# Performance work log

Hardware: AMD Instinct MI355X
Metric: run time of the kernel (lower is better)

Reference implementation:

```python
import jax, jax.numpy as jnp
import numpy as np

C = 64
G = 4          # group_number
K = 3          # kernel_size
R = 4          # reduction_ratio -> bottleneck C//R = 16
BN_EPS = 1e-3  # keras BatchNormalization default epsilon


def setup_inputs() -> dict:
    key = jax.random.key(0)
    ks = jax.random.split(key, 8)
    B, H, W = 8, 192, 192
    cr = C // R
    x = jax.random.normal(ks[0], (B, H, W, C), dtype=jnp.float32)
    # kernel_gen: Conv2D 1x1 (C -> C//R), BN, ReLU, Conv2D 1x1 (C//R -> K*K*G)
    w1 = jax.random.normal(ks[1], (C, cr), dtype=jnp.float32) * (1.0 / np.sqrt(C))
    b1 = jnp.zeros((cr,), dtype=jnp.float32)
    gamma = 1.0 + 0.1 * jax.random.normal(ks[2], (cr,), dtype=jnp.float32)
    beta = 0.1 * jax.random.normal(ks[3], (cr,), dtype=jnp.float32)
    mean = 0.1 * jax.random.normal(ks[4], (cr,), dtype=jnp.float32)
    var = jax.random.uniform(ks[5], (cr,), dtype=jnp.float32, minval=0.5, maxval=1.5)
    w2 = jax.random.normal(ks[6], (cr, K * K * G), dtype=jnp.float32) * (1.0 / np.sqrt(cr))
    b2 = jnp.zeros((K * K * G,), dtype=jnp.float32)
    return {"x": x, "w1": w1, "b1": b1, "gamma": gamma, "beta": beta,
            "mean": mean, "var": var, "w2": w2, "b2": b2}


def reference(x, w1, b1, gamma, beta, mean, var, w2, b2):
    B, H, W, Cc = x.shape
    # --- kernel generation (stride=1 -> identity pooling) ---
    t = jnp.einsum('bhwc,cd->bhwd', x, w1) + b1                 # [B,H,W,C//R]
    t = (t - mean) * jax.lax.rsqrt(var + BN_EPS) * gamma + beta  # BN (inference)
    t = jax.nn.relu(t)
    kern = jnp.einsum('bhwd,de->bhwe', t, w2) + b2               # [B,H,W,K*K*G]
    kern = kern.reshape(B, H, W, K * K, 1, G)
    # --- unfold: tf.image.extract_patches SAME, stride 1, patch order (ki,kj,C) ---
    pad = K // 2
    xp = jnp.pad(x, ((0, 0), (pad, pad), (pad, pad), (0, 0)))
    patches = jnp.stack(
        [xp[:, i:i + H, j:j + W, :] for i in range(K) for j in range(K)],
        axis=3)                                                  # [B,H,W,K*K,C]
    unfolded = patches.reshape(B, H, W, K * K, Cc // G, G)
    # --- per-pixel multiply-reduce over patch axis ---
    out = jnp.sum(kern * unfolded, axis=3)                       # [B,H,W,C//G,G]
    return out.reshape(B, H, W, Cc)
```

## Files before the change

kernel.cpp:

```cpp
#include <hip/hip_runtime.h>


#define B_   8
#define H_   192
#define W_   192
#define C_   64
#define CR_  16
#define TH_  8
#define TW_  16
#define TILES_X (W_/TW_)
#define TILES_Y (H_/TH_)
#define TILES_PER_IMG (TILES_X * TILES_Y)
#define NBLK (B_ * TILES_PER_IMG)
#define NPIX (TH_ * TW_)

constexpr float BN_EPS = 1e-3f;

template <bool INTERIOR>
__device__ __forceinline__ void phase_b(const float* __restrict__ x,
                                        float* __restrict__ out,
                                        const float4* __restrict__ s_kern,
                                        int img, int th0, int tw0, int tid)
{
    const int c4i  = tid & 15;
    const int prow = tid >> 4;
    const float* ximg = x + ((size_t)img * H_ * W_ << 6);
    float* oimg = out + ((size_t)img * H_ * W_ << 6);

    #pragma unroll 2
    for (int i = 0; i < 16; ++i) {
        const int q = i * 8 + prow;
        const int r = q >> 4, cc = q & 15;
        const int h = th0 + r, w = tw0 + cc;
        const float4* kq = &s_kern[q * 9];

        float4 acc = make_float4(0.f, 0.f, 0.f, 0.f);
        #pragma unroll
        for (int ti = 0; ti < 3; ++ti) {
            const int hh = h + ti - 1;
            int hc = hh;
            bool vh = true;
            if (!INTERIOR) {
                vh = (unsigned)hh < (unsigned)H_;
                hc = hh < 0 ? 0 : (hh >= H_ ? H_ - 1 : hh);
            }
            #pragma unroll
            for (int tj = 0; tj < 3; ++tj) {
                const int ww = w + tj - 1;
                int wc = ww;
                bool valid = true;
                if (!INTERIOR) {
                    valid = vh && ((unsigned)ww < (unsigned)W_);
                    wc = ww < 0 ? 0 : (ww >= W_ ? W_ - 1 : ww);
                }
                const float4 xv = reinterpret_cast<const float4*>(
                    ximg + ((size_t)(hc * W_ + wc) << 6))[c4i];
                float4 kv = kq[ti * 3 + tj];
                if (!INTERIOR) {
                    kv.x = valid ? kv.x : 0.f;
                    kv.y = valid ? kv.y : 0.f;
                    kv.z = valid ? kv.z : 0.f;
                    kv.w = valid ? kv.w : 0.f;
                }
                acc.x = fmaf(kv.x, xv.x, acc.x);
                acc.y = fmaf(kv.y, xv.y, acc.y);
                acc.z = fmaf(kv.z, xv.z, acc.z);
                acc.w = fmaf(kv.w, xv.w, acc.w);
            }
        }
        reinterpret_cast<float4*>(oimg + ((size_t)(h * W_ + w) << 6))[c4i] = acc;
    }
}

__global__ __launch_bounds__(128, 4)
void invol_fused(const float* __restrict__ x,
                 const float* __restrict__ w1,
                 const float* __restrict__ b1,
                 const float* __restrict__ gamma,
                 const float* __restrict__ beta,
                 const float* __restrict__ mean,
                 const float* __restrict__ var,
                 const float* __restrict__ w2,
                 const float* __restrict__ b2,
                 float* __restrict__ out)
{
    __shared__ float4 s_kern[NPIX * 9];

    const int bid = blockIdx.x;
    const int img = bid & 7;
    const int tin = bid >> 3;
    const int th0 = (tin / TILES_X) * TH_;
    const int tw0 = (tin % TILES_X) * TW_;

    const int tid = threadIdx.x;

    {
        const int r = tid >> 4, cc = tid & 15;
        const int h = th0 + r, w = tw0 + cc;
        const float4* xp = reinterpret_cast<const float4*>(
            x + ((size_t)((img * H_ + h) * W_ + w) << 6));

        float td[CR_];
        #pragma unroll
        for (int d = 0; d < CR_; ++d) td[d] = 0.f;

        #pragma unroll
        for (int c4 = 0; c4 < 16; ++c4) {
            const float4 xv = xp[c4];
            const float xs[4] = {xv.x, xv.y, xv.z, xv.w};
            #pragma unroll
            for (int k = 0; k < 4; ++k) {
                const float* wr = w1 + (c4 * 4 + k) * CR_;
                #pragma unroll
                for (int d = 0; d < CR_; ++d)
                    td[d] = fmaf(xs[k], wr[d], td[d]);
            }
        }

        #pragma unroll
        for (int d = 0; d < CR_; ++d) {
            const float a = gamma[d] * rsqrtf(var[d] + BN_EPS);
            const float c = (b1[d] - mean[d]) * a + beta[d];
            td[d] = fmaxf(fmaf(td[d], a, c), 0.f);
        }

        float ke[36];
        #pragma unroll
        for (int e = 0; e < 36; ++e) ke[e] = b2[e];
        #pragma unroll
        for (int d = 0; d < CR_; ++d) {
            const float t = td[d];
            const float* wr = w2 + d * 36;
            #pragma unroll
            for (int e = 0; e < 36; ++e)
                ke[e] = fmaf(t, wr[e], ke[e]);
        }

        float4* skq = &s_kern[tid * 9];
        #pragma unroll
        for (int t9 = 0; t9 < 9; ++t9)
            skq[t9] = make_float4(ke[t9 * 4 + 0], ke[t9 * 4 + 1],
                                  ke[t9 * 4 + 2], ke[t9 * 4 + 3]);
    }

    __syncthreads();

    const bool interior = (th0 > 0) && (th0 + TH_ < H_) &&
                          (tw0 > 0) && (tw0 + TW_ < W_);
    if (interior)
        phase_b<true>(x, out, s_kern, img, th0, tw0, tid);
    else
        phase_b<false>(x, out, s_kern, img, th0, tw0, tid);
}

extern "C" void kernel_launch(void* const* d_in, const int* in_sizes, int n_in,
                              void* d_out, int out_size, void* d_ws, size_t ws_size,
                              hipStream_t stream) {
    const float* x     = (const float*)d_in[0];
    const float* w1    = (const float*)d_in[1];
    const float* b1    = (const float*)d_in[2];
    const float* gamma = (const float*)d_in[3];
    const float* beta  = (const float*)d_in[4];
    const float* mean  = (const float*)d_in[5];
    const float* var   = (const float*)d_in[6];
    const float* w2    = (const float*)d_in[7];
    const float* b2    = (const float*)d_in[8];
    float* out = (float*)d_out;

    invol_fused<<<dim3(NBLK), dim3(128), 0, stream>>>(
        x, w1, b1, gamma, beta, mean, var, w2, b2, out);
}
```

Measured before the change: 201.3 us.

## Split kernel generation across four threads per pixel with 8x8 tiles

Tiles shrink from 8x16 to 8x8 pixels and blocks grow to 256 threads, so each pixel's kernel-generation MLP is now split across 4 threads (4 bottleneck channels each, then 9 of the 36 kernel weights each). A shared-memory staging buffer for the bottleneck activations and an extra barrier are added. The aim is to cut per-thread register pressure and serial FMA chains in the generation phase and raise occupancy. The cost is more blocks, more halo reloads per output, and the added synchronization.

```diff
diff --git a/kernel.cpp b/kernel.cpp
--- a/kernel.cpp
+++ b/kernel.cpp
@@ -4,15 +4,13 @@
 #define B_   8
 #define H_   192
 #define W_   192
-#define C_   64
 #define CR_  16
 #define TH_  8
-#define TW_  16
+#define TW_  8
 #define TILES_X (W_/TW_)
-#define TILES_Y (H_/TH_)
-#define TILES_PER_IMG (TILES_X * TILES_Y)
-#define NBLK (B_ * TILES_PER_IMG)
-#define NPIX (TH_ * TW_)
+#define TILES_PER_IMG (TILES_X*(H_/TH_))
+#define NBLK (B_*TILES_PER_IMG)
+#define NPIX (TH_*TW_)
 
 constexpr float BN_EPS = 1e-3f;
 
@@ -22,39 +20,41 @@
                                         const float4* __restrict__ s_kern,
                                         int img, int th0, int tw0, int tid)
 {
-    const int c4i  = tid & 15;
-    const int prow = tid >> 4;
-    const float* ximg = x + ((size_t)img * H_ * W_ << 6);
-    float* oimg = out + ((size_t)img * H_ * W_ << 6);
+    const int lane = tid & 63;
+    const int wv   = tid >> 6;
+    const int ploc = lane >> 4;
+    const int c4i  = lane & 15;
+    const float* ximg = x + (((size_t)(img * H_ * W_)) << 6);
+    float* oimg = out + (((size_t)(img * H_ * W_)) << 6);
 
-    #pragma unroll 2
-    for (int i = 0; i < 16; ++i) {
-        const int q = i * 8 + prow;
-        const int r = q >> 4, cc = q & 15;
-        const int h = th0 + r, w = tw0 + cc;
-        const float4* kq = &s_kern[q * 9];
+    #pragma unroll
+    for (int i = 0; i < 4; ++i) {
+        const int Q   = wv * 4 + i;
+        const int row = Q >> 1, qc = Q & 1;
+        const int h   = th0 + row;
+        const int w   = tw0 + qc * 4 + ploc;
+        const int px  = row * 8 + qc * 4 + ploc;
+        const float4* kq = &s_kern[px * 9];
 
         float4 acc = make_float4(0.f, 0.f, 0.f, 0.f);
         #pragma unroll
         for (int ti = 0; ti < 3; ++ti) {
-            const int hh = h + ti - 1;
-            int hc = hh;
+            int hh = h + ti - 1;
             bool vh = true;
             if (!INTERIOR) {
                 vh = (unsigned)hh < (unsigned)H_;
-                hc = hh < 0 ? 0 : (hh >= H_ ? H_ - 1 : hh);
+                hh = hh < 0 ? 0 : (hh >= H_ ? H_ - 1 : hh);
             }
             #pragma unroll
             for (int tj = 0; tj < 3; ++tj) {
-                const int ww = w + tj - 1;
-                int wc = ww;
-                bool valid = true;
+                int ww = w + tj - 1;
+                bool valid = vh;
                 if (!INTERIOR) {
                     valid = vh && ((unsigned)ww < (unsigned)W_);
-                    wc = ww < 0 ? 0 : (ww >= W_ ? W_ - 1 : ww);
+                    ww = ww < 0 ? 0 : (ww >= W_ ? W_ - 1 : ww);
                 }
                 const float4 xv = reinterpret_cast<const float4*>(
-                    ximg + ((size_t)(hc * W_ + wc) << 6))[c4i];
+                    ximg + (((size_t)(hh * W_ + ww)) << 6))[c4i];
                 float4 kv = kq[ti * 3 + tj];
                 if (!INTERIOR) {
                     kv.x = valid ? kv.x : 0.f;
@@ -68,11 +68,11 @@
                 acc.w = fmaf(kv.w, xv.w, acc.w);
             }
         }
-        reinterpret_cast<float4*>(oimg + ((size_t)(h * W_ + w) << 6))[c4i] = acc;
+        reinterpret_cast<float4*>(oimg + (((size_t)(h * W_ + w)) << 6))[c4i] = acc;
     }
 }
 
-__global__ __launch_bounds__(128, 4)
+__global__ __launch_bounds__(256, 8)
 void invol_fused(const float* __restrict__ x,
                  const float* __restrict__ w1,
                  const float* __restrict__ b1,
@@ -84,7 +84,8 @@
                  const float* __restrict__ b2,
                  float* __restrict__ out)
 {
-    __shared__ float4 s_kern[NPIX * 9];
+    __shared__ float4 s_t4[NPIX * 4];
+    __shared__ float4 s_kern4[NPIX * 9];
 
     const int bid = blockIdx.x;
     const int img = bid & 7;
@@ -93,64 +94,71 @@
     const int tw0 = (tin % TILES_X) * TW_;
 
     const int tid = threadIdx.x;
+    const int px  = tid >> 2;
+    const int sub = tid & 3;
+    const int r = px >> 3, cc = px & 7;
+    const int h = th0 + r, w = tw0 + cc;
 
     {
-        const int r = tid >> 4, cc = tid & 15;
-        const int h = th0 + r, w = tw0 + cc;
         const float4* xp = reinterpret_cast<const float4*>(
-            x + ((size_t)((img * H_ + h) * W_ + w) << 6));
+            x + (((size_t)((img * H_ + h) * W_ + w)) << 6));
 
-        float td[CR_];
-        #pragma unroll
-        for (int d = 0; d < CR_; ++d) td[d] = 0.f;
-
+        float td[4] = {0.f, 0.f, 0.f, 0.f};
         #pragma unroll
         for (int c4 = 0; c4 < 16; ++c4) {
             const float4 xv = xp[c4];
             const float xs[4] = {xv.x, xv.y, xv.z, xv.w};
             #pragma unroll
             for (int k = 0; k < 4; ++k) {
-                const float* wr = w1 + (c4 * 4 + k) * CR_;
-                #pragma unroll
-                for (int d = 0; d < CR_; ++d)
-                    td[d] = fmaf(xs[k], wr[d], td[d]);
+                const float4 wv4 = reinterpret_cast<const float4*>(
+                    w1 + (c4 * 4 + k) * CR_)[sub];
+                td[0] = fmaf(xs[k], wv4.x, td[0]);
+                td[1] = fmaf(xs[k], wv4.y, td[1]);
+                td[2] = fmaf(xs[k], wv4.z, td[2]);
+                td[3] = fmaf(xs[k], wv4.w, td[3]);
             }
         }
-
         #pragma unroll
-        for (int d = 0; d < CR_; ++d) {
-            const float a = gamma[d] * rsqrtf(var[d] + BN_EPS);
-            const float c = (b1[d] - mean[d]) * a + beta[d];
+        for (int d = 0; d < 4; ++d) {
+            const int dd = sub * 4 + d;
+            const float a = gamma[dd] * rsqrtf(var[dd] + BN_EPS);
+            const float c = (b1[dd] - mean[dd]) * a + beta[dd];
             td[d] = fmaxf(fmaf(td[d], a, c), 0.f);
         }
+        s_t4[px * 4 + sub] = make_float4(td[0], td[1], td[2], td[3]);
+    }
+    __syncthreads();
 
-        float ke[36];
+    {
+        float t[16];
         #pragma unroll
-        for (int e = 0; e < 36; ++e) ke[e] = b2[e];
+        for (int k = 0; k < 4; ++k) {
+            const float4 tq = s_t4[px * 4 + k];
+            t[k * 4 + 0] = tq.x; t[k * 4 + 1] = tq.y;
+            t[k * 4 + 2] = tq.z; t[k * 4 + 3] = tq.w;
+        }
+        float ke[9];
         #pragma unroll
-        for (int d = 0; d < CR_; ++d) {
-            const float t = td[d];
-            const float* wr = w2 + d * 36;
+        for (int j = 0; j < 9; ++j) ke[j] = b2[sub * 9 + j];
+        #pragma unroll
+        for (int d = 0; d < 16; ++d) {
+            const float* wr = w2 + d * 36 + sub * 9;
             #pragma unroll
-            for (int e = 0; e < 36; ++e)
-                ke[e] = fmaf(t, wr[e], ke[e]);
+            for (int j = 0; j < 9; ++j)
+                ke[j] = fmaf(t[d], wr[j], ke[j]);
         }
-
-        float4* skq = &s_kern[tid * 9];
+        float* sk = reinterpret_cast<float*>(s_kern4) + px * 36 + sub * 9;
         #pragma unroll
-        for (int t9 = 0; t9 < 9; ++t9)
-            skq[t9] = make_float4(ke[t9 * 4 + 0], ke[t9 * 4 + 1],
-                                  ke[t9 * 4 + 2], ke[t9 * 4 + 3]);
+        for (int j = 0; j < 9; ++j) sk[j] = ke[j];
     }
-
     __syncthreads();
 
     const bool interior = (th0 > 0) && (th0 + TH_ < H_) &&
                           (tw0 > 0) && (tw0 + TW_ < W_);
     if (interior)
-        phase_b<true>(x, out, s_kern, img, th0, tw0, tid);
+        phase_b<true>(x, out, s_kern4, img, th0, tw0, tid);
     else
-        phase_b<false>(x, out, s_kern, img, th0, tw0, tid);
+        phase_b<false>(x, out, s_kern4, img, th0, tw0, tid);
 }
 
 extern "C" void kernel_launch(void* const* d_in, const int* in_sizes, int n_in,
@@ -167,6 +175,6 @@
     const float* b2    = (const float*)d_in[8];
     float* out = (float*)d_out;
 
-    invol_fused<<<dim3(NBLK), dim3(128), 0, stream>>>(
+    invol_fused<<<dim3(NBLK), dim3(256), 0, stream>>>(
         x, w1, b1, gamma, beta, mean, var, w2, b2, out);
 }
```

New measurement: 233.8 us. +16.1%, slower.
